# Optimization experiments

Measured on AMD Instinct MI355X. Metric: run time of the kernel, lower is better.

## Reference

```python
import jax, jax.numpy as jnp
import numpy as np

EPSILON = 0.01
RHO_X = 5.0
MAX_ITER_OUTER = 5
MAX_ITER_INNER = 100

N, D1 = 4096, 128
M, D2 = 4096, 128


def setup_inputs() -> dict:
    key = jax.random.key(0)
    kx, ky = jax.random.split(key)
    X = jax.random.normal(kx, (N, D1), dtype=jnp.float32)
    Y = jax.random.normal(ky, (M, D2), dtype=jnp.float32)
    return {"X": X, "Y": Y}


def _coot_cost_samples(X, Y, pi_f):
    # pi_f: [d1, d2] -> cost over samples [N, M]
    r = jnp.sum(pi_f, axis=1)            # [d1]
    c = jnp.sum(pi_f, axis=0)            # [d2]
    t1 = (X * X) @ r                     # [N]
    t2 = (Y * Y) @ c                     # [M]
    cross = -2.0 * (X @ pi_f @ Y.T)      # [N, M]
    return t1[:, None] + t2[None, :] + cross


def _coot_cost_features(X, Y, pi_s):
    # pi_s: [N, M] -> cost over features [d1, d2]
    r = jnp.sum(pi_s, axis=1)            # [N]
    c = jnpp.sum(pi_s, axis=0) if False else jnp.sum(pi_s, axis=0)  # [M]
    t1 = (X * X).T @ r                   # [d1]
    t2 = (Y * Y).T @ c                   # [d2]
    cross = -2.0 * (X.T @ pi_s @ Y)      # [d1, d2]
    return t1[:, None] + t2[None, :] + cross


def _s_uot_sinkhorn(C, mu, nu, gamma):
    # min-max normalize C (guard degenerate flat cost)
    c_min = C.min()
    c_max = C.max()
    scale = c_max - c_min
    safe = jnp.where(scale > 1e-8, scale, jnp.float32(1.0))
    C_norm = jnp.where(scale > 1e-8, (C - c_min) / safe, jnp.zeros_like(C))
    K = jnp.exp(-C_norm / EPSILON)

    def step(b, _):
        a = (mu / (K @ b + 1e-16)) ** gamma
        b_new = nu / (K.T @ a + 1e-16)   # is_balanced_nu=True in both calls
        return b_new, a

    b0 = jnp.ones_like(nu)
    b, a_hist = jax.lax.scan(step, b0, None, length=MAX_ITER_INNER)
    a = a_hist[-1]
    # diag(a) @ K @ diag(b) without materializing diagonals
    return a[:, None] * K * b[None, :]


def reference(X, Y):
    n, d1 = X.shape
    m, d2 = Y.shape
    mu_s = jnp.full((n,), 1.0 / n, dtype=X.dtype)
    nu_s = jnp.full((m,), 1.0 / m, dtype=X.dtype)
    mu_f = jnp.full((d1,), 1.0 / d1, dtype=X.dtype)
    nu_f = jnp.full((d2,), 1.0 / d2, dtype=X.dtype)

    pi_f = mu_f[:, None] * nu_f[None, :]
    gamma_s = RHO_X / (RHO_X + EPSILON)

    pi_s = mu_s[:, None] * nu_s[None, :]
    for _ in range(MAX_ITER_OUTER):
        C_s = _coot_cost_samples(X, Y, pi_f)
        pi_s_new = _s_uot_sinkhorn(C_s, mu_s, nu_s, gamma_s)
        pi_s = pi_s_new * (pi_f.sum() / (pi_s_new.sum() + 1e-16))

        C_f = _coot_cost_features(X, Y, pi_s)
        pi_f_new = _s_uot_sinkhorn(C_f, mu_f, nu_f, jnp.float32(1.0))
        pi_f = pi_f_new * (pi_s.sum() / (pi_f_new.sum() + 1e-16))

    return (pi_s, pi_f)
```

## Files before the change

kernel.cpp:

```cpp
#include <hip/hip_runtime.h>
#include <math.h>
#include <cfloat>

#define NROW 4096
#define DFEAT 128
constexpr float EPS32   = 0.01f;
constexpr float GAMMA32 = (float)(5.0/5.01);
constexpr float MU_S    = 1.0f/4096.0f;
constexpr float MU_F    = 1.0f/128.0f;
constexpr float TINY    = 1e-16f;


__device__ __forceinline__ float sepf(float x){ asm volatile("" : "+v"(x)); return x; }


__device__ __forceinline__ float np_leaf128(const float* a){
    float r0=a[0],r1=a[1],r2=a[2],r3=a[3],r4=a[4],r5=a[5],r6=a[6],r7=a[7];
    #pragma unroll
    for (int i=8;i<128;i+=8){
        r0+=a[i+0]; r1+=a[i+1]; r2+=a[i+2]; r3+=a[i+3];
        r4+=a[i+4]; r5+=a[i+5]; r6+=a[i+6]; r7+=a[i+7];
    }
    return ((r0+r1)+(r2+r3)) + ((r4+r5)+(r6+r7));
}

__device__ __forceinline__ float blas_dot128(const float* x, const float* y){
    float acc[8];
    #pragma unroll
    for (int p=0;p<8;p++) acc[p]=0.f;
    #pragma unroll
    for (int m=0;m<16;m++)
        #pragma unroll
        for (int p=0;p<8;p++) acc[p] = fmaf(x[m*8+p], y[m*8+p], acc[p]);
    float s0=acc[0]+acc[4], s1=acc[1]+acc[5], s2=acc[2]+acc[6], s3=acc[3]+acc[7];
    return (s0+s1)+(s2+s3);
}


__global__ void k_fill(float* __restrict__ p, int n, float v){
    int i = blockIdx.x*blockDim.x + threadIdx.x;
    if (i < n) p[i] = v;
}

__global__ __launch_bounds__(128) void k_pifsums(const float* __restrict__ pif,
        float* __restrict__ rvec, float* __restrict__ cvec, float* __restrict__ scal){
    int t = threadIdx.x;
    float rs = np_leaf128(pif + t*DFEAT);
    rvec[t] = rs;
    float cs = pif[t];
    for (int i=1;i<DFEAT;i++) cs += pif[i*DFEAT + t];
    cvec[t] = cs;
    __shared__ float ld[128];
    ld[t] = rs; __syncthreads();
    for (int h=64; h>=1; h>>=1){
        if (t<h) ld[t] = ld[2*t] + ld[2*t+1];
        __syncthreads();
    }
    if (t==0) scal[0] = ld[0];
}

__global__ __launch_bounds__(256) void k_tvec(const float* __restrict__ M,
        const float* __restrict__ r, float* __restrict__ out){
    int row = blockIdx.x*32 + (threadIdx.x >> 3);
    int p   = threadIdx.x & 7;
    const float* mr = M + (size_t)row*DFEAT;
    float acc = 0.f;
    #pragma unroll
    for (int m=0;m<16;m++){
        float x = mr[p + 8*m];
        float xx = x*x;
        acc = fmaf(xx, r[p + 8*m], acc);
    }
    acc += __shfl_xor(acc, 4);
    acc += __shfl_xor(acc, 1);
    acc += __shfl_xor(acc, 2);
    if (p==0) out[row] = acc;
}

__global__ __launch_bounds__(256) void k_gemm_w(const float* __restrict__ X,
        const float* __restrict__ pif, float* __restrict__ W){
    int o = blockIdx.x*256 + threadIdx.x;
    int i = o >> 7, j = o & 127;
    const float* xr = X + (size_t)i*DFEAT;
    float acc = 0.f;
    #pragma unroll 8
    for (int k=0;k<DFEAT;k++) acc = fmaf(xr[k], pif[k*DFEAT + j], acc);
    W[o] = acc;
}

__global__ __launch_bounds__(256) void k_gemm_c(const float* __restrict__ W, const float* __restrict__ Y,
        const float* __restrict__ t1, const float* __restrict__ t2,
        float* __restrict__ C, float* __restrict__ bmin, float* __restrict__ bmax){
    __shared__ float Ws[16][132];
    __shared__ float Ys[16][132];
    int t = threadIdx.x;
    int bi = blockIdx.y, bj = blockIdx.x;
    for (int l=t; l<2048; l+=256){
        int r = l>>7, k = l&127;
        Ws[r][k] = W[(size_t)(bi*16+r)*DFEAT + k];
        Ys[r][k] = Y[(size_t)(bj*16+r)*DFEAT + k];
    }
    __syncthreads();
    int a = t >> 4, b = t & 15;
    float acc = 0.f;
    #pragma unroll 8
    for (int k=0;k<DFEAT;k++) acc = fmaf(Ws[a][k], Ys[b][k], acc);
    int gi = bi*16 + a, gj = bj*16 + b;
    float t12 = t1[gi] + t2[gj];
    float v   = t12 + (-2.0f*acc);
    C[(size_t)gi*NROW + gj] = v;
    __shared__ float rmn[256], rmx[256];
    rmn[t]=v; rmx[t]=v; __syncthreads();
    for (int s=128;s;s>>=1){
        if (t<s){ rmn[t]=fminf(rmn[t],rmn[t+s]); rmx[t]=fmaxf(rmx[t],rmx[t+s]); }
        __syncthreads();
    }
    if (t==0){ int bid = bi*gridDim.x + bj; bmin[bid]=rmn[0]; bmax[bid]=rmx[0]; }
}

__global__ void k_minmax(const float* __restrict__ bmin, const float* __restrict__ bmax,
                         int n, float* __restrict__ scal){
    int t = threadIdx.x;
    float mn=FLT_MAX, mx=-FLT_MAX;
    for (int i=t;i<n;i+=256){ mn=fminf(mn,bmin[i]); mx=fmaxf(mx,bmax[i]); }
    __shared__ float rmn[256], rmx[256];
    rmn[t]=mn; rmx[t]=mx; __syncthreads();
    for (int s=128;s;s>>=1){
        if (t<s){ rmn[t]=fminf(rmn[t],rmn[t+s]); rmx[t]=fmaxf(rmx[t],rmx[t+s]); }
        __syncthreads();
    }
    if (t==0){
        float cmin=rmn[0], scale=rmx[0]-rmn[0];
        scal[1]=cmin;
        scal[2]=(scale>1e-8f)? scale : 1.0f;
        scal[3]=(scale>1e-8f)? 1.0f  : 0.0f;
    }
}

__global__ void k_exp(float* __restrict__ K, const float* __restrict__ scal){
    float cmin=scal[1], safe=scal[2], flag=scal[3];
    int stride = gridDim.x*blockDim.x;
    for (int i = blockIdx.x*blockDim.x+threadIdx.x; i < NROW*NROW; i += stride){
        if (flag > 0.5f){
            float sub = K[i] - cmin;
            float cn  = sub / safe;
            float arg = (-cn) / EPS32;
            K[i] = (float)exp((double)arg);
        } else {
            K[i] = 1.0f;
        }
    }
}

__global__ __launch_bounds__(256) void k_exp_t(float* __restrict__ K, float* __restrict__ KT,
        const float* __restrict__ scal){
    __shared__ float tile[64][65];
    float cmin=scal[1], safe=scal[2], flag=scal[3];
    int bi = blockIdx.y, bj = blockIdx.x;
    int t = threadIdx.x;
    for (int l=t; l<4096; l+=256){
        int r = l>>6, c = l&63;
        size_t idx = (size_t)(bi*64+r)*NROW + bj*64+c;
        float v = K[idx];
        if (flag > 0.5f){
            float sub = v - cmin;
            float cn  = sub / safe;
            float arg = (-cn) / EPS32;
            v = (float)exp((double)arg);
        } else v = 1.0f;
        K[idx] = v;
        tile[c][r] = v;
    }
    __syncthreads();
    for (int l=t; l<4096; l+=256){
        int r = l>>6, c = l&63;
        KT[(size_t)(bj*64+r)*NROW + bi*64+c] = tile[r][c];
    }
}

__global__ __launch_bounds__(128) void k_kb_np(const float* __restrict__ K,
        const float* __restrict__ bv, float* __restrict__ av){
    int row = blockIdx.x*16 + (threadIdx.x >> 3);
    int p   = threadIdx.x & 7;
    const float* Kr = K + (size_t)row*NROW;
    float acc = 0.f;
    #pragma unroll 16
    for (int m=0;m<512;m++) acc = fmaf(Kr[p+8*m], bv[p+8*m], acc);
    acc += __shfl_xor(acc, 4);
    acc += __shfl_xor(acc, 1);
    acc += __shfl_xor(acc, 2);
    if (p==0){
        float den = acc + TINY;
        float q   = MU_S / den;
        av[row] = (float)pow((double)q, (double)GAMMA32);
    }
}

__global__ __launch_bounds__(256) void k_kta_np(const float* __restrict__ K,
        const float* __restrict__ av, float* __restrict__ kta, float* __restrict__ bv){
    int j = blockIdx.x*256 + threadIdx.x;
    float s = 0.f;
    #pragma unroll 4
    for (int i=0;i<NROW;i++) s = fmaf(av[i], K[(size_t)i*NROW + j], s);
    kta[j] = s;
    bv[j]  = MU_S/(s + TINY);
}

__global__ __launch_bounds__(64) void k_kta_fast(const float* __restrict__ KT,
        const float* __restrict__ av, float* __restrict__ kta, float* __restrict__ bv){
    int j = blockIdx.x*64 + threadIdx.x;
    const float4* row = reinterpret_cast<const float4*>(KT + (size_t)j*NROW);
    float s = 0.f;
    #pragma unroll 16
    for (int i4=0; i4<1024; i4++){
        float4 kv = row[i4];
        s = fmaf(av[i4*4+0], kv.x, s);
        s = fmaf(av[i4*4+1], kv.y, s);
        s = fmaf(av[i4*4+2], kv.z, s);
        s = fmaf(av[i4*4+3], kv.w, s);
    }
    kta[j] = s;
    bv[j]  = MU_S/(s + TINY);
}

__global__ __launch_bounds__(64) void k_leafs_pisnew(const float* __restrict__ K,
        const float* __restrict__ av, const float* __restrict__ bv, float* __restrict__ leafS){
    int lane = threadIdx.x;
    int row  = blockIdx.x*2 + (lane>>5);
    int L    = lane & 31;
    float a  = av[row];
    const float* Kr = K + (size_t)row*NROW + L*128;
    const float* br = bv + L*128;
    float r0,r1,r2,r3,r4,r5,r6,r7;
    r0=sepf((a*Kr[0])*br[0]); r1=sepf((a*Kr[1])*br[1]);
    r2=sepf((a*Kr[2])*br[2]); r3=sepf((a*Kr[3])*br[3]);
    r4=sepf((a*Kr[4])*br[4]); r5=sepf((a*Kr[5])*br[5]);
    r6=sepf((a*Kr[6])*br[6]); r7=sepf((a*Kr[7])*br[7]);
    #pragma unroll
    for (int i=8;i<128;i+=8){
        r0+=sepf((a*Kr[i+0])*br[i+0]); r1+=sepf((a*Kr[i+1])*br[i+1]);
        r2+=sepf((a*Kr[i+2])*br[i+2]); r3+=sepf((a*Kr[i+3])*br[i+3]);
        r4+=sepf((a*Kr[i+4])*br[i+4]); r5+=sepf((a*Kr[i+5])*br[i+5]);
        r6+=sepf((a*Kr[i+6])*br[i+6]); r7+=sepf((a*Kr[i+7])*br[i+7]);
    }
    leafS[row*32 + L] = ((r0+r1)+(r2+r3)) + ((r4+r5)+(r6+r7));
}

__global__ __launch_bounds__(128) void k_tree1(const float* __restrict__ leafS,
        float* __restrict__ part){
    __shared__ float ld[256];
    int t = threadIdx.x, g = blockIdx.x;
    ld[t]     = leafS[g*256 + t];
    ld[t+128] = leafS[g*256 + t + 128];
    __syncthreads();
    for (int h=128; h>=1; h>>=1){
        if (t<h) ld[t] = ld[2*t] + ld[2*t+1];
        __syncthreads();
    }
    if (t==0) part[g] = ld[0];
}

template<int MODE>
__global__ __launch_bounds__(256) void k_tree2(const float* __restrict__ part,
        float* __restrict__ scal){
    __shared__ float ld[512];
    int t = threadIdx.x;
    ld[t]     = part[t];
    ld[t+256] = part[t+256];
    __syncthreads();
    for (int h=256; h>=1; h>>=1){
        if (t<h) ld[t] = ld[2*t] + ld[2*t+1];
        __syncthreads();
    }
    if (t==0){
        float S = ld[0];
        if (MODE==0) scal[4] = scal[0]/(S + TINY);
        else         scal[5] = S;
    }
}

__global__ void k_finalize(float* __restrict__ K, const float* __restrict__ av,
        const float* __restrict__ bv, const float* __restrict__ scal){
    float ratio = scal[4];
    int stride = gridDim.x*blockDim.x;
    for (int idx = blockIdx.x*blockDim.x+threadIdx.x; idx < NROW*NROW; idx += stride){
        int row = idx >> 12, col = idx & 4095;
        K[idx] = ((av[row]*K[idx])*bv[col])*ratio;
    }
}

__global__ __launch_bounds__(64) void k_rows_np(const float* __restrict__ P,
        float* __restrict__ rsf, float* __restrict__ leafS){
    int lane = threadIdx.x;
    int row  = blockIdx.x*2 + (lane>>5);
    int L    = lane & 31;
    float leaf = np_leaf128(P + (size_t)row*NROW + L*128);
    leafS[row*32 + L] = leaf;
    float s = leaf;
    s += __shfl_xor(s, 1);
    s += __shfl_xor(s, 2);
    s += __shfl_xor(s, 4);
    s += __shfl_xor(s, 8);
    s += __shfl_xor(s, 16);
    if (L==0) rsf[row] = s;
}

__global__ __launch_bounds__(256) void k_cols_np(const float* __restrict__ P,
        float* __restrict__ csf){
    int j = blockIdx.x*256 + threadIdx.x;
    float s = P[j];
    #pragma unroll 4
    for (int i=1;i<NROW;i++) s += P[(size_t)i*NROW + j];
    csf[j] = s;
}

__global__ __launch_bounds__(64) void k_cols_fast(const float* __restrict__ KT,
        const float* __restrict__ av, const float* __restrict__ bv,
        const float* __restrict__ scal, float* __restrict__ csf){
    int j = blockIdx.x*64 + threadIdx.x;
    float b = bv[j], ratio = scal[4];
    const float4* row = reinterpret_cast<const float4*>(KT + (size_t)j*NROW);
    float s = 0.f;
    #pragma unroll 8
    for (int i4=0; i4<1024; i4++){
        float4 kv = row[i4];
        s += ((av[i4*4+0]*kv.x)*b)*ratio;
        s += ((av[i4*4+1]*kv.y)*b)*ratio;
        s += ((av[i4*4+2]*kv.z)*b)*ratio;
        s += ((av[i4*4+3]*kv.w)*b)*ratio;
    }
    csf[j] = s;
}

__global__ __launch_bounds__(128) void k_tvec_f(const float* __restrict__ M,
        const float* __restrict__ r, float* __restrict__ out){
    int k = threadIdx.x;
    float s = 0.f;
    #pragma unroll 8
    for (int i=0;i<NROW;i++){
        float x = M[(size_t)i*DFEAT + k];
        float xx = x*x;
        s = fmaf(xx, r[i], s);
    }
    out[k] = s;
}

__global__ __launch_bounds__(256) void k_U(const float* __restrict__ X,
        const float* __restrict__ P, float* __restrict__ U){
    int o = blockIdx.x*256 + threadIdx.x;
    int j = o & 4095, k = o >> 12;
    float acc = 0.f;
    for (int t=0; t<11; t++){
        int i0 = t*384;
        int len = (i0+384 <= NROW) ? 384 : (NROW - i0);
        float part = 0.f;
        #pragma unroll 4
        for (int q=0;q<len;q++)
            part = fmaf(X[(size_t)(i0+q)*DFEAT + k], P[(size_t)(i0+q)*NROW + j], part);
        acc = (t==0) ? part : acc + part;
    }
    U[(size_t)k*NROW + j] = acc;
}

__global__ __launch_bounds__(64) void k_U_fast(const float* __restrict__ X,
        const float* __restrict__ KT, const float* __restrict__ av,
        const float* __restrict__ bv, const float* __restrict__ scal,
        float* __restrict__ U){
    int j  = (blockIdx.x >> 3)*64 + threadIdx.x;
    int k0 = (blockIdx.x & 7)*16;
    float b = bv[j], ratio = scal[4];
    const float* ktrow = KT + (size_t)j*NROW;
    float acc[16];
    for (int t=0; t<11; t++){
        int i0 = t*384;
        int len = (i0+384 <= NROW) ? 384 : (NROW - i0);
        float part[16];
        #pragma unroll
        for (int d=0;d<16;d++) part[d]=0.f;
        #pragma unroll 4
        for (int q=0;q<len;q++){
            float kt = ktrow[i0+q];
            float p  = ((av[i0+q]*kt)*b)*ratio;
            const float* xr = X + (size_t)(i0+q)*DFEAT + k0;
            #pragma unroll
            for (int d=0;d<16;d++) part[d] = fmaf(xr[d], p, part[d]);
        }
        #pragma unroll
        for (int d=0;d<16;d++) acc[d] = (t==0)? part[d] : acc[d]+part[d];
    }
    #pragma unroll
    for (int d=0;d<16;d++) U[(size_t)(k0+d)*NROW + j] = acc[d];
}

__global__ __launch_bounds__(256) void k_V(const float* __restrict__ U,
        const float* __restrict__ Y, const float* __restrict__ t1f,
        const float* __restrict__ t2f, float* __restrict__ Cf){
    int o = blockIdx.x*256 + threadIdx.x;
    int k = o >> 7, l = o & 127;
    float acc = 0.f;
    for (int t=0; t<11; t++){
        int j0 = t*384;
        int len = (j0+384 <= NROW) ? 384 : (NROW - j0);
        float part = 0.f;
        #pragma unroll 4
        for (int q=0;q<len;q++)
            part = fmaf(U[(size_t)k*NROW + j0+q], Y[(size_t)(j0+q)*DFEAT + l], part);
        acc = (t==0) ? part : acc + part;
    }
    float t12 = t1f[k] + t2f[l];
    Cf[o] = t12 + (-2.0f*acc);
}

__global__ __launch_bounds__(128) void k_sinkhorn_f_np(const float* __restrict__ Cf,
        const float* __restrict__ scal, float* __restrict__ pif){
    __shared__ float kf[128][129];
    __shared__ float a_s[128], b_s[128];
    __shared__ float red[128];
    __shared__ float cmin_sh, safe_sh, flag_sh, fsc_sh;
    int t = threadIdx.x;
    for (int idx=t; idx<16384; idx+=128) kf[idx>>7][idx&127] = Cf[idx];
    __syncthreads();
    float mn = kf[t][0], mx = kf[t][0];
    for (int c=1;c<128;c++){ float v=kf[t][c]; mn=fminf(mn,v); mx=fmaxf(mx,v); }
    red[t]=mn; __syncthreads();
    for (int s=64;s;s>>=1){ if(t<s) red[t]=fminf(red[t],red[t+s]); __syncthreads(); }
    if (t==0) cmin_sh = red[0];
    __syncthreads();
    red[t]=mx; __syncthreads();
    for (int s=64;s;s>>=1){ if(t<s) red[t]=fmaxf(red[t],red[t+s]); __syncthreads(); }
    if (t==0){
        float scale = red[0] - cmin_sh;
        safe_sh = (scale>1e-8f)? scale : 1.0f;
        flag_sh = (scale>1e-8f)? 1.0f  : 0.0f;
    }
    __syncthreads();
    float cmin=cmin_sh, safe=safe_sh, flag=flag_sh;
    for (int c=0;c<128;c++){
        if (flag > 0.5f){
            float sub = kf[t][c] - cmin;
            float cn  = sub / safe;
            float arg = (-cn) / EPS32;
            kf[t][c]  = (float)exp((double)arg);
        } else kf[t][c] = 1.0f;
    }
    b_s[t] = 1.0f;
    __syncthreads();
    float x[128];
    #pragma unroll 4
    for (int c=0;c<128;c++) x[c] = kf[t][c];
    for (int it=0; it<100; it++){
        float kb = blas_dot128(x, b_s);
        a_s[t] = MU_F/(kb + TINY);
        __syncthreads();
        float s = 0.f;
        #pragma unroll 4
        for (int i=0;i<128;i++) s = fmaf(a_s[i], kf[i][t], s);
        b_s[t] = MU_F/(s + TINY);
        __syncthreads();
    }
    float ar = a_s[t];
    float e[128];
    #pragma unroll 4
    for (int c=0;c<128;c++) e[c] = sepf((ar*x[c])*b_s[c]);
    {
        float r0=e[0],r1=e[1],r2=e[2],r3=e[3],r4=e[4],r5=e[5],r6=e[6],r7=e[7];
        #pragma unroll
        for (int i=8;i<128;i+=8){
            r0+=e[i+0]; r1+=e[i+1]; r2+=e[i+2]; r3+=e[i+3];
            r4+=e[i+4]; r5+=e[i+5]; r6+=e[i+6]; r7+=e[i+7];
        }
        red[t] = ((r0+r1)+(r2+r3)) + ((r4+r5)+(r6+r7));
    }
    __syncthreads();
    for (int h=64; h>=1; h>>=1){
        if (t<h) red[t] = red[2*t] + red[2*t+1];
        __syncthreads();
    }
    if (t==0) fsc_sh = scal[5]/(red[0] + TINY);
    __syncthreads();
    float fsc = fsc_sh;
    #pragma unroll 4
    for (int c=0;c<128;c++) pif[t*DFEAT + c] = e[c]*fsc;
}

extern "C" void kernel_launch(void* const* d_in, const int* in_sizes, int n_in,
                              void* d_out, int out_size, void* d_ws, size_t ws_size,
                              hipStream_t stream){
    const float* X = (const float*)d_in[0];
    const float* Y = (const float*)d_in[1];
    float* out  = (float*)d_out;
    float* Kmat = out;
    float* pif  = out + (size_t)NROW*NROW;
    float* w = (float*)d_ws;
    float* W      = w;
    float* U      = W      + 524288;
    float* leafS  = U      + 524288;
    float* part   = leafS  + 131072;
    float* av     = part   + 512;
    float* bv     = av     + 4096;
    float* kta    = bv     + 4096;
    float* rsf    = kta    + 4096;
    float* csf    = rsf    + 4096;
    float* t1     = csf    + 4096;
    float* t2     = t1     + 4096;
    float* bmin   = t2     + 4096;
    float* bmax   = bmin   + 65536;
    float* rvec   = bmax   + 65536;
    float* cvec   = rvec   + 128;
    float* t1f    = cvec   + 128;
    float* t2f    = t1f    + 128;
    float* Cf     = t2f    + 128;
    float* scal   = Cf     + 16384;
    float* KT     = scal   + 16;
    size_t need_floats = (size_t)(KT - w) + (size_t)NROW*NROW;
    bool hasKT = ws_size >= need_floats*sizeof(float);

    k_fill<<<64, 256, 0, stream>>>(pif, 16384, 1.0f/16384.0f);
    for (int outer=0; outer<5; outer++){
        k_pifsums<<<1, 128, 0, stream>>>(pif, rvec, cvec, scal);
        k_tvec<<<128, 256, 0, stream>>>(X, rvec, t1);
        k_tvec<<<128, 256, 0, stream>>>(Y, cvec, t2);
        k_gemm_w<<<2048, 256, 0, stream>>>(X, pif, W);
        k_gemm_c<<<dim3(256,256), 256, 0, stream>>>(W, Y, t1, t2, Kmat, bmin, bmax);
        k_minmax<<<1, 256, 0, stream>>>(bmin, bmax, 65536, scal);
        if (hasKT) k_exp_t<<<dim3(64,64), 256, 0, stream>>>(Kmat, KT, scal);
        else       k_exp<<<2048, 256, 0, stream>>>(Kmat, scal);
        k_fill<<<16, 256, 0, stream>>>(bv, 4096, 1.0f);
        for (int it=0; it<100; it++){
            k_kb_np<<<256, 128, 0, stream>>>(Kmat, bv, av);
            if (hasKT) k_kta_fast<<<64, 64, 0, stream>>>(KT, av, kta, bv);
            else       k_kta_np<<<16, 256, 0, stream>>>(Kmat, av, kta, bv);
        }
        k_leafs_pisnew<<<2048, 64, 0, stream>>>(Kmat, av, bv, leafS);
        k_tree1<<<512, 128, 0, stream>>>(leafS, part);
        k_tree2<0><<<1, 256, 0, stream>>>(part, scal);
        k_finalize<<<2048, 256, 0, stream>>>(Kmat, av, bv, scal);
        k_rows_np<<<2048, 64, 0, stream>>>(Kmat, rsf, leafS);
        k_tree1<<<512, 128, 0, stream>>>(leafS, part);
        k_tree2<1><<<1, 256, 0, stream>>>(part, scal);
        if (hasKT) k_cols_fast<<<64, 64, 0, stream>>>(KT, av, bv, scal, csf);
        else       k_cols_np<<<16, 256, 0, stream>>>(Kmat, csf);
        k_tvec_f<<<1, 128, 0, stream>>>(X, rsf, t1f);
        k_tvec_f<<<1, 128, 0, stream>>>(Y, csf, t2f);
        if (hasKT) k_U_fast<<<512, 64, 0, stream>>>(X, KT, av, bv, scal, U);
        else       k_U<<<2048, 256, 0, stream>>>(X, Kmat, U);
        k_V<<<64, 256, 0, stream>>>(U, Y, t1f, t2f, Cf);
        k_sinkhorn_f_np<<<1, 128, 0, stream>>>(Cf, scal, pif);
    }
}
```

Baseline: 42.15 ms.

## Stage Sinkhorn vectors in LDS and software-pipeline KT row loads in K^T·a

The K·b kernel now copies the whole b vector into shared memory and drops to 64-thread blocks with deeper unrolling. The K^T·a kernel stages a into LDS and keeps four register buffers of 16 float4 loads each, refilling one while computing on another, to hide global memory latency. That kernel has only 64 single-wave blocks, so the aim is more memory parallelism per wave, paid for with heavy register use. A sepf barrier is added in the column-sum kernel, apparently to pin the floating-point rounding order rather than for speed.

```diff
diff --git a/kernel.cpp b/kernel.cpp
--- a/kernel.cpp
+++ b/kernel.cpp
@@ -178,14 +178,22 @@
     }
 }
 
-__global__ __launch_bounds__(128) void k_kb_np(const float* __restrict__ K,
+__global__ __launch_bounds__(64) void k_kb_np(const float* __restrict__ K,
         const float* __restrict__ bv, float* __restrict__ av){
-    int row = blockIdx.x*16 + (threadIdx.x >> 3);
-    int p   = threadIdx.x & 7;
+    __shared__ float bvs[NROW];
+    int t = threadIdx.x;
+    {
+        float4* d = reinterpret_cast<float4*>(bvs);
+        const float4* s4 = reinterpret_cast<const float4*>(bv);
+        for (int i=t;i<1024;i+=64) d[i] = s4[i];
+    }
+    __syncthreads();
+    int row = blockIdx.x*8 + (t>>3);
+    int p   = t & 7;
     const float* Kr = K + (size_t)row*NROW;
     float acc = 0.f;
-    #pragma unroll 16
-    for (int m=0;m<512;m++) acc = fmaf(Kr[p+8*m], bv[p+8*m], acc);
+    #pragma unroll 32
+    for (int m=0;m<512;m++) acc = fmaf(Kr[p+8*m], bvs[p+8*m], acc);
     acc += __shfl_xor(acc, 4);
     acc += __shfl_xor(acc, 1);
     acc += __shfl_xor(acc, 2);
@@ -206,18 +214,67 @@
     bv[j]  = MU_S/(s + TINY);
 }
 
-__global__ __launch_bounds__(64) void k_kta_fast(const float* __restrict__ KT,
+__global__ __launch_bounds__(64,1) void k_kta_fast(const float* __restrict__ KT,
         const float* __restrict__ av, float* __restrict__ kta, float* __restrict__ bv){
-    int j = blockIdx.x*64 + threadIdx.x;
+    __shared__ float avs[NROW];
+    int t = threadIdx.x;
+    float4* avs4 = reinterpret_cast<float4*>(avs);
+    {
+        const float4* s4 = reinterpret_cast<const float4*>(av);
+        for (int i=t;i<1024;i+=64) avs4[i] = s4[i];
+    }
+    __syncthreads();
+    int j = blockIdx.x*64 + t;
     const float4* row = reinterpret_cast<const float4*>(KT + (size_t)j*NROW);
+    float4 A[16], B[16], C[16], D[16];
+    #pragma unroll
+    for (int k=0;k<16;k++) A[k]=row[k];
+    #pragma unroll
+    for (int k=0;k<16;k++) B[k]=row[16+k];
+    #pragma unroll
+    for (int k=0;k<16;k++) C[k]=row[32+k];
+    #pragma unroll
+    for (int k=0;k<16;k++) D[k]=row[48+k];
     float s = 0.f;
-    #pragma unroll 16
-    for (int i4=0; i4<1024; i4++){
-        float4 kv = row[i4];
-        s = fmaf(av[i4*4+0], kv.x, s);
-        s = fmaf(av[i4*4+1], kv.y, s);
-        s = fmaf(av[i4*4+2], kv.z, s);
-        s = fmaf(av[i4*4+3], kv.w, s);
+    #pragma unroll 1
+    for (int it=0; it<16; it++){
+        int b0 = it*64;
+        #pragma unroll
+        for (int k=0;k<16;k++){
+            float4 a4 = avs4[b0+k]; float4 v = A[k];
+            s=fmaf(a4.x,v.x,s); s=fmaf(a4.y,v.y,s); s=fmaf(a4.z,v.z,s); s=fmaf(a4.w,v.w,s);
+        }
+        if (it<15){
+            #pragma unroll
+            for (int k=0;k<16;k++) A[k]=row[b0+64+k];
+        }
+        #pragma unroll
+        for (int k=0;k<16;k++){
+            float4 a4 = avs4[b0+16+k]; float4 v = B[k];
+            s=fmaf(a4.x,v.x,s); s=fmaf(a4.y,v.y,s); s=fmaf(a4.z,v.z,s); s=fmaf(a4.w,v.w,s);
+        }
+        if (it<15){
+            #pragma unroll
+            for (int k=0;k<16;k++) B[k]=row[b0+80+k];
+        }
+        #pragma unroll
+        for (int k=0;k<16;k++){
+            float4 a4 = avs4[b0+32+k]; float4 v = C[k];
+            s=fmaf(a4.x,v.x,s); s=fmaf(a4.y,v.y,s); s=fmaf(a4.z,v.z,s); s=fmaf(a4.w,v.w,s);
+        }
+        if (it<15){
+            #pragma unroll
+            for (int k=0;k<16;k++) C[k]=row[b0+96+k];
+        }
+        #pragma unroll
+        for (int k=0;k<16;k++){
+            float4 a4 = avs4[b0+48+k]; float4 v = D[k];
+            s=fmaf(a4.x,v.x,s); s=fmaf(a4.y,v.y,s); s=fmaf(a4.z,v.z,s); s=fmaf(a4.w,v.w,s);
+        }
+        if (it<15){
+            #pragma unroll
+            for (int k=0;k<16;k++) D[k]=row[b0+112+k];
+        }
     }
     kta[j] = s;
     bv[j]  = MU_S/(s + TINY);
@@ -324,10 +381,10 @@
     #pragma unroll 8
     for (int i4=0; i4<1024; i4++){
         float4 kv = row[i4];
-        s += ((av[i4*4+0]*kv.x)*b)*ratio;
-        s += ((av[i4*4+1]*kv.y)*b)*ratio;
-        s += ((av[i4*4+2]*kv.z)*b)*ratio;
-        s += ((av[i4*4+3]*kv.w)*b)*ratio;
+        s += sepf(((av[i4*4+0]*kv.x)*b)*ratio);
+        s += sepf(((av[i4*4+1]*kv.y)*b)*ratio);
+        s += sepf(((av[i4*4+2]*kv.z)*b)*ratio);
+        s += sepf(((av[i4*4+3]*kv.w)*b)*ratio);
     }
     csf[j] = s;
 }
@@ -527,7 +584,7 @@
         else       k_exp<<<2048, 256, 0, stream>>>(Kmat, scal);
         k_fill<<<16, 256, 0, stream>>>(bv, 4096, 1.0f);
         for (int it=0; it<100; it++){
-            k_kb_np<<<256, 128, 0, stream>>>(Kmat, bv, av);
+            k_kb_np<<<512, 64, 0, stream>>>(Kmat, bv, av);
             if (hasKT) k_kta_fast<<<64, 64, 0, stream>>>(KT, av, kta, bv);
             else       k_kta_np<<<16, 256, 0, stream>>>(Kmat, av, kta, bv);
         }
```

New measurement: 113.4 ms. +169.0%, slower.

## Stage KT columns and av in LDS with many blocks for the K^T a step

Applied to the files above, without the earlier changes.

Replaces the 64-block K^T·a kernel, where each thread streamed its own 16KB row with uncoalesced global loads, with a 1024-block kernel. Each block cooperatively loads four KT rows and the av vector into shared memory with coalesced float4 loads. A single lane per wave then does the sequential FMA chain, keeping the original summation order. The aim is to spread the bandwidth-bound inner Sinkhorn step across far more CUs, at the cost of about 80KB of LDS per block and a serial per-lane reduction. Separately, the column-sum kernel now wraps each product in sepf, which blocks FMA contraction and keeps the rounding order fixed.

```diff
diff --git a/kernel.cpp b/kernel.cpp
--- a/kernel.cpp
+++ b/kernel.cpp
@@ -206,21 +206,36 @@
     bv[j]  = MU_S/(s + TINY);
 }
 
-__global__ __launch_bounds__(64) void k_kta_fast(const float* __restrict__ KT,
+__global__ __launch_bounds__(256) void k_kta_blk(const float* __restrict__ KT,
         const float* __restrict__ av, float* __restrict__ kta, float* __restrict__ bv){
-    int j = blockIdx.x*64 + threadIdx.x;
-    const float4* row = reinterpret_cast<const float4*>(KT + (size_t)j*NROW);
-    float s = 0.f;
-    #pragma unroll 16
-    for (int i4=0; i4<1024; i4++){
-        float4 kv = row[i4];
-        s = fmaf(av[i4*4+0], kv.x, s);
-        s = fmaf(av[i4*4+1], kv.y, s);
-        s = fmaf(av[i4*4+2], kv.z, s);
-        s = fmaf(av[i4*4+3], kv.w, s);
-    }
-    kta[j] = s;
-    bv[j]  = MU_S/(s + TINY);
+    __shared__ float buf[4][NROW];
+    __shared__ float avs[NROW];
+    int t = threadIdx.x;
+    int j0 = blockIdx.x*4;
+    {
+        const float4* av4 = reinterpret_cast<const float4*>(av);
+        float4* a4 = reinterpret_cast<float4*>(avs);
+        #pragma unroll
+        for (int i=t;i<1024;i+=256) a4[i] = av4[i];
+        #pragma unroll
+        for (int c=0;c<4;c++){
+            const float4* r4 = reinterpret_cast<const float4*>(KT + (size_t)(j0+c)*NROW);
+            float4* b4 = reinterpret_cast<float4*>(&buf[c][0]);
+            #pragma unroll
+            for (int i=t;i<1024;i+=256) b4[i] = r4[i];
+        }
+    }
+    __syncthreads();
+    int w = t >> 6, lane = t & 63;
+    if (lane==0){
+        const float* bc = &buf[w][0];
+        float s = 0.f;
+        #pragma unroll 8
+        for (int i=0;i<NROW;i++) s = fmaf(avs[i], bc[i], s);
+        int j = j0 + w;
+        kta[j] = s;
+        bv[j]  = MU_S/(s + TINY);
+    }
 }
 
 __global__ __launch_bounds__(64) void k_leafs_pisnew(const float* __restrict__ K,
@@ -324,10 +339,10 @@
     #pragma unroll 8
     for (int i4=0; i4<1024; i4++){
         float4 kv = row[i4];
-        s += ((av[i4*4+0]*kv.x)*b)*ratio;
-        s += ((av[i4*4+1]*kv.y)*b)*ratio;
-        s += ((av[i4*4+2]*kv.z)*b)*ratio;
-        s += ((av[i4*4+3]*kv.w)*b)*ratio;
+        s += sepf(((av[i4*4+0]*kv.x)*b)*ratio);
+        s += sepf(((av[i4*4+1]*kv.y)*b)*ratio);
+        s += sepf(((av[i4*4+2]*kv.z)*b)*ratio);
+        s += sepf(((av[i4*4+3]*kv.w)*b)*ratio);
     }
     csf[j] = s;
 }
@@ -528,7 +543,7 @@
         k_fill<<<16, 256, 0, stream>>>(bv, 4096, 1.0f);
         for (int it=0; it<100; it++){
             k_kb_np<<<256, 128, 0, stream>>>(Kmat, bv, av);
-            if (hasKT) k_kta_fast<<<64, 64, 0, stream>>>(KT, av, kta, bv);
+            if (hasKT) k_kta_blk<<<1024, 256, 0, stream>>>(KT, av, kta, bv);
             else       k_kta_np<<<16, 256, 0, stream>>>(Kmat, av, kta, bv);
         }
         k_leafs_pisnew<<<2048, 64, 0, stream>>>(Kmat, av, bv, leafS);
```

Result: slower. 69.55 ms (+65.0%).
